# Optimization experiments

Hardware: AMD Instinct MI355X
Metric: run time of the kernel (lower is better)

## Reference

```python
import jax, jax.numpy as jnp
import numpy as np

BLOCK_H = 32
BLOCK_W = 32
HEADS = 16
SEQ = 1024
BATCH = 8
HEAD_DIM = 64


def _block_mask(mask):
    # conv with all-ones kernel, stride = block size, grouped per head == block sum-pool, then >0
    H, S, Sw = mask.shape
    nb_h, nb_w = S // BLOCK_H, Sw // BLOCK_W
    pooled = mask.reshape(H, nb_h, BLOCK_H, nb_w, BLOCK_W).sum(axis=(2, 4))
    return pooled > 0  # [H, nb_h, nb_w] bool


def setup_inputs() -> dict:
    key = jax.random.key(0)
    kq, kk, kv, km = jax.random.split(key, 4)
    q = jax.random.normal(kq, (BATCH, HEADS, SEQ, HEAD_DIM), dtype=jnp.float32)
    k = jax.random.normal(kk, (BATCH, HEADS, SEQ, HEAD_DIM), dtype=jnp.float32)
    v = jax.random.normal(kv, (BATCH, HEADS, SEQ, HEAD_DIM), dtype=jnp.float32)
    # with diagonal blocks always present (valid causal layout, matches triton usage).
    nb = SEQ // BLOCK_H
    bm = jax.random.uniform(km, (HEADS, nb, nb)) < 0.25
    bm = bm | jnp.eye(nb, dtype=bool)[None, :, :]
    # expand block mask to element-level float mask [H, S, S]
    mask = jnp.broadcast_to(
        bm[:, :, None, :, None], (HEADS, nb, BLOCK_H, nb, BLOCK_W)
    ).reshape(HEADS, SEQ, SEQ).astype(jnp.float32)
    return {"query": q, "key": k, "value": v, "mask": mask}


def reference(query, key, value, mask):
    scale = 1.0
    bm = _block_mask(mask)  # [H, nb, nb]
    nb = bm.shape[-1]
    # expand block layout back to element granularity (triton masks per-block only)
    elem = jnp.broadcast_to(
        bm[:, :, None, :, None], (bm.shape[0], nb, BLOCK_H, nb, BLOCK_W)
    ).reshape(bm.shape[0], nb * BLOCK_H, nb * BLOCK_W)
    causal = jnp.tril(jnp.ones((elem.shape[-2], elem.shape[-1]), dtype=bool))
    full = elem & causal[None]  # [H, S, S]
    # SDD: QK^T only on layout blocks; dense equivalent masks to -inf elsewhere
    scores = jnp.einsum("bhqd,bhkd->bhqk", query, key) * scale
    scores = jnp.where(full[None], scores, -jnp.inf)
    probs = jax.nn.softmax(scores, axis=-1)  # every row has a valid diagonal-block entry
    # DSD: sparse probs @ dense V
    out = jnp.einsum("bhqk,bhkd->bhqd", probs, value)
    return out
```

## Files before the change

kernel.cpp:

```cpp
#include <hip/hip_runtime.h>
#include <stdint.h>

typedef unsigned short u16;
typedef short bf16x8 __attribute__((ext_vector_type(8)));
typedef bf16x8 __attribute__((may_alias)) bf16x8_a;
typedef unsigned u32x2 __attribute__((ext_vector_type(2)));
typedef u32x2 __attribute__((may_alias)) u32x2_a;
typedef float f32x4 __attribute__((ext_vector_type(4)));
typedef f32x4 __attribute__((may_alias)) f32x4_a;

#define BATCH 8
#define HEADS 16
#define SEQ 1024
#define HD 64
#define NB 32
#define LOG2E 1.44269504f
#define MBIAS 46.16624128f
#define BLK 2048

__device__ unsigned g_bm[HEADS * NB];
__device__ u16 g_kb[(size_t)BATCH * HEADS * NB * BLK];
__device__ u16 g_kl[(size_t)BATCH * HEADS * NB * BLK];
__device__ u16 g_vt[(size_t)BATCH * HEADS * NB * BLK];

__device__ __forceinline__ u16 f2bf(float x) {
    unsigned u = __builtin_bit_cast(unsigned, x);
    u += 0x7fffu + ((u >> 16) & 1u);
    return (u16)(u >> 16);
}
__device__ __forceinline__ float bf2f(u16 h) {
    unsigned u = ((unsigned)h) << 16;
    return __builtin_bit_cast(float, u);
}
__device__ __forceinline__ bf16x8 pack8(float4 a, float4 b) {
    bf16x8 r;
    r[0] = (short)f2bf(a.x); r[1] = (short)f2bf(a.y);
    r[2] = (short)f2bf(a.z); r[3] = (short)f2bf(a.w);
    r[4] = (short)f2bf(b.x); r[5] = (short)f2bf(b.y);
    r[6] = (short)f2bf(b.z); r[7] = (short)f2bf(b.w);
    return r;
}
__device__ __forceinline__ bf16x8 pack8_res(float4 a, float4 b, bf16x8 hi) {
    bf16x8 r;
    r[0] = (short)f2bf(a.x - bf2f((u16)hi[0])); r[1] = (short)f2bf(a.y - bf2f((u16)hi[1]));
    r[2] = (short)f2bf(a.z - bf2f((u16)hi[2])); r[3] = (short)f2bf(a.w - bf2f((u16)hi[3]));
    r[4] = (short)f2bf(b.x - bf2f((u16)hi[4])); r[5] = (short)f2bf(b.y - bf2f((u16)hi[5]));
    r[6] = (short)f2bf(b.z - bf2f((u16)hi[6])); r[7] = (short)f2bf(b.w - bf2f((u16)hi[7]));
    return r;
}

__global__ __launch_bounds__(256) void prep_kv(const float* __restrict__ k,
                                               const float* __restrict__ v,
                                               const float* __restrict__ mask) {
    __shared__ float tile[64 * 65];
    int bid = blockIdx.x;
    int t = threadIdx.x;
    if (bid < 4096) {
        int bh = bid >> 5, j = bid & 31;
        int row = t >> 3, dg = t & 7;
        const float* s = k + ((size_t)(bh * SEQ + j * 32 + row)) * HD + dg * 8;
        float4 a = *(const float4*)(s);
        float4 b = *(const float4*)(s + 4);
        bf16x8 hi = pack8(a, b);
        bf16x8 lo = pack8_res(a, b, hi);
        int c = ((row >> 4) << 1) + (dg >> 2);
        int lane = (row & 15) + ((dg & 3) << 4);
        size_t o = ((size_t)(bh * NB + j)) * BLK + c * 512 + lane * 8;
        *(bf16x8*)(g_kb + o) = hi;
        *(bf16x8*)(g_kl + o) = lo;
        return;
    }
    if (bid < 6144) {
        int tb = bid - 4096;
        int bh = tb >> 4, kt = tb & 15;
        const float* src = v + ((size_t)(bh * SEQ + kt * 64)) * HD;
#pragma unroll
        for (int p = 0; p < 4; ++p) {
            int row = p * 16 + (t >> 4);
            int col = (t & 15) * 4;
            float4 d = *(const float4*)(src + (size_t)row * HD + col);
            float* tp = &tile[row * 65 + col];
            tp[0] = d.x; tp[1] = d.y; tp[2] = d.z; tp[3] = d.w;
        }
        __syncthreads();
#pragma unroll
        for (int p = 0; p < 2; ++p) {
            int dd = p * 32 + (t >> 3);
            int kc = (t & 7) * 8;
            u16 tmp[8];
#pragma unroll
            for (int i = 0; i < 8; ++i) tmp[i] = f2bf(tile[(kc + i) * 65 + dd]);
            int j = kt * 2 + (kc >> 5);
            int kk = kc & 31;
            int c = dd >> 4;
            int lane = (dd & 15) + ((kk >> 3) << 4);
            size_t o = ((size_t)(bh * NB + j)) * BLK + c * 512 + lane * 8;
            *(uint4*)(g_vt + o) = *(const uint4*)tmp;
        }
        return;
    }
    int h = bid - 6144;
    int lane = t & 63;
#pragma unroll
    for (int kk2 = 0; kk2 < 4; ++kk2) {
        int tt = (kk2 << 8) | t;
        int i = tt >> 5, j = tt & 31;
        float mv = mask[(size_t)h * SEQ * SEQ + (size_t)(i * 32) * SEQ + (size_t)(j * 32)];
        bool pred = (j == i) || (j < i && mv != 0.0f);
        unsigned long long bal = __ballot(pred);
        if (lane == 0)  g_bm[h * NB + i] = (unsigned)(bal & 0xffffffffull);
        if (lane == 32) g_bm[h * NB + i] = (unsigned)(bal >> 32);
    }
}

__device__ __forceinline__ void load_blk(size_t kb, bf16x8 (&kh)[4], bf16x8 (&kl)[4],
                                         bf16x8 (&vf)[4]) {
#pragma unroll
    for (int c = 0; c < 4; ++c) {
        kh[c] = *(const bf16x8_a*)(const void*)(g_kb + kb + c * 512);
        kl[c] = *(const bf16x8_a*)(const void*)(g_kl + kb + c * 512);
        vf[c] = *(const bf16x8_a*)(const void*)(g_vt + kb + c * 512);
    }
}

__device__ __forceinline__ void compute_blk(int j, int i32, int qcol, int quad,
                                            const bf16x8 (&kh)[4], const bf16x8 (&kl)[4],
                                            const bf16x8 (&vf)[4],
                                            const bf16x8 (&qh)[2][2], const bf16x8 (&ql)[2][2],
                                            u16* pl, f32x4 (&oacc)[2][4], float& l0, float& l1) {
    f32x4 tt[2][2];
    __builtin_amdgcn_s_setprio(1);
#pragma unroll
    for (int kt = 0; kt < 2; ++kt)
#pragma unroll
        for (int t = 0; t < 2; ++t) {
            f32x4 acc = f32x4{0.f, 0.f, 0.f, 0.f};
            acc = __builtin_amdgcn_mfma_f32_16x16x32_bf16(kl[kt*2+0], qh[t][0], acc, 0, 0, 0);
            acc = __builtin_amdgcn_mfma_f32_16x16x32_bf16(kl[kt*2+1], qh[t][1], acc, 0, 0, 0);
            acc = __builtin_amdgcn_mfma_f32_16x16x32_bf16(kh[kt*2+0], ql[t][0], acc, 0, 0, 0);
            acc = __builtin_amdgcn_mfma_f32_16x16x32_bf16(kh[kt*2+1], ql[t][1], acc, 0, 0, 0);
            acc = __builtin_amdgcn_mfma_f32_16x16x32_bf16(kh[kt*2+0], qh[t][0], acc, 0, 0, 0);
            acc = __builtin_amdgcn_mfma_f32_16x16x32_bf16(kh[kt*2+1], qh[t][1], acc, 0, 0, 0);
            tt[kt][t] = acc;
        }
    __builtin_amdgcn_s_setprio(0);

    if (j == i32) {
#pragma unroll
        for (int kt = 0; kt < 2; ++kt)
#pragma unroll
            for (int t = 0; t < 2; ++t)
#pragma unroll
                for (int r = 0; r < 4; ++r) {
                    int key = kt * 16 + quad * 4 + r;
                    if (key > t * 16 + qcol) tt[kt][t][r] = -1e30f;
                }
    }

    u16 pb[2][8];
#pragma unroll
    for (int kt = 0; kt < 2; ++kt)
#pragma unroll
        for (int t = 0; t < 2; ++t) {
            float psum = 0.f;
#pragma unroll
            for (int r = 0; r < 4; ++r) {
                float e = exp2f(tt[kt][t][r] * LOG2E - MBIAS);
                u16 eb = f2bf(e);
                pb[t][kt * 4 + r] = eb;
                psum += bf2f(eb);
            }
            if (t == 0) l0 += psum; else l1 += psum;
        }

#pragma unroll
    for (int t = 0; t < 2; ++t)
#pragma unroll
        for (int kt = 0; kt < 2; ++kt) {
            u32x2 pw;
            pw[0] = (unsigned)pb[t][kt*4+0] | ((unsigned)pb[t][kt*4+1] << 16);
            pw[1] = (unsigned)pb[t][kt*4+2] | ((unsigned)pb[t][kt*4+3] << 16);
            *(u32x2_a*)(pl + (t * 16 + qcol) * 40 + kt * 16 + quad * 4) = pw;
        }
    bf16x8 pf0 = *(const bf16x8_a*)(pl + qcol * 40 + quad * 8);
    bf16x8 pf1 = *(const bf16x8_a*)(pl + (16 + qcol) * 40 + quad * 8);

    __builtin_amdgcn_s_setprio(1);
#pragma unroll
    for (int c = 0; c < 4; ++c) {
        oacc[0][c] = __builtin_amdgcn_mfma_f32_16x16x32_bf16(vf[c], pf0, oacc[0][c], 0, 0, 0);
        oacc[1][c] = __builtin_amdgcn_mfma_f32_16x16x32_bf16(vf[c], pf1, oacc[1][c], 0, 0, 0);
    }
    __builtin_amdgcn_s_setprio(0);
}

__global__ __launch_bounds__(128) void attn(const float* __restrict__ q,
                                            float* __restrict__ out) {
    __shared__ __align__(16) u16 pbuf[2][1280];
    __shared__ __align__(16) float mbuf[2176];
    __shared__ float lbuf[2][16];

    int w = threadIdx.x >> 6;
    int lane = threadIdx.x & 63;
    int qcol = lane & 15;
    int quad = lane >> 4;

    int bid = blockIdx.x;
    int slot = bid & 7;
    int r = bid >> 3;
    int half = r >> 8;
    int rr = r & 255;
    int i32 = 31 - (rr >> 3);
    int bh = slot + ((((half << 3) | (rr & 7))) << 3);
    int h = bh & (HEADS - 1);

    bf16x8 qh[2][2], ql[2][2];
#pragma unroll
    for (int t = 0; t < 2; ++t) {
        const float* qb = q + ((size_t)(bh * SEQ + i32 * 32 + t * 16 + qcol)) * HD + quad * 8;
#pragma unroll
        for (int dh = 0; dh < 2; ++dh) {
            float4 a = *(const float4*)(qb + dh * 32);
            float4 b = *(const float4*)(qb + dh * 32 + 4);
            qh[t][dh] = pack8(a, b);
            ql[t][dh] = pack8_res(a, b, qh[t][dh]);
        }
    }

    unsigned bits = g_bm[h * NB + i32];
    unsigned mybits = 0;
    {
        unsigned b = bits; int c = 0;
        while (b) { int j = __builtin_ctz(b); b &= b - 1; if ((c & 1) == w) mybits |= (1u << j); ++c; }
    }

    size_t bhbase = (size_t)bh * NB * BLK + lane * 8;
    u16* pl = pbuf[w];

    f32x4 oacc[2][4];
#pragma unroll
    for (int t = 0; t < 2; ++t)
#pragma unroll
        for (int c = 0; c < 4; ++c) oacc[t][c] = f32x4{0.f, 0.f, 0.f, 0.f};
    float l0 = 0.f, l1 = 0.f;

    bf16x8 khA[4], klA[4], vfA[4], khB[4], klB[4], vfB[4];
    unsigned rem = mybits;
    if (rem) {
        int jA = __builtin_ctz(rem); rem &= rem - 1;
        load_blk(bhbase + (size_t)jA * BLK, khA, klA, vfA);
        for (;;) {
            int jB = -1;
            if (rem) { jB = __builtin_ctz(rem); rem &= rem - 1;
                       load_blk(bhbase + (size_t)jB * BLK, khB, klB, vfB); }
            compute_blk(jA, i32, qcol, quad, khA, klA, vfA, qh, ql, pl, oacc, l0, l1);
            if (jB < 0) break;
            jA = -1;
            if (rem) { jA = __builtin_ctz(rem); rem &= rem - 1;
                       load_blk(bhbase + (size_t)jA * BLK, khA, klA, vfA); }
            compute_blk(jB, i32, qcol, quad, khB, klB, vfB, qh, ql, pl, oacc, l0, l1);
            if (jA < 0) break;
        }
    }

    l0 += __shfl_xor(l0, 16); l0 += __shfl_xor(l0, 32);
    l1 += __shfl_xor(l1, 16); l1 += __shfl_xor(l1, 32);

    if (w == 1) {
#pragma unroll
        for (int t = 0; t < 2; ++t)
#pragma unroll
            for (int c = 0; c < 4; ++c) {
                f32x4 val;
                val[0] = oacc[t][c][0]; val[1] = oacc[t][c][1];
                val[2] = oacc[t][c][2]; val[3] = oacc[t][c][3];
                *(f32x4_a*)(&mbuf[(t * 16 + qcol) * 68 + c * 16 + quad * 4]) = val;
            }
        if (quad == 0) { lbuf[0][qcol] = l0; lbuf[1][qcol] = l1; }
    }
    __syncthreads();
    if (w == 0) {
        float inv[2];
        inv[0] = 1.0f / (l0 + lbuf[0][qcol]);
        inv[1] = 1.0f / (l1 + lbuf[1][qcol]);
#pragma unroll
        for (int t = 0; t < 2; ++t)
#pragma unroll
            for (int c = 0; c < 4; ++c) {
                float* mp = &mbuf[(t * 16 + qcol) * 68 + c * 16 + quad * 4];
                f32x4 o = *(const f32x4_a*)mp;
                o[0] = (o[0] + oacc[t][c][0]) * inv[t];
                o[1] = (o[1] + oacc[t][c][1]) * inv[t];
                o[2] = (o[2] + oacc[t][c][2]) * inv[t];
                o[3] = (o[3] + oacc[t][c][3]) * inv[t];
                *(f32x4_a*)mp = o;
            }
    }
    __syncthreads();
    float* obase = out + ((size_t)(bh * SEQ + i32 * 32)) * HD;
#pragma unroll
    for (int g2 = 0; g2 < 4; ++g2) {
        int gr = w * 4 + g2;
        int row = gr * 4 + (lane >> 4);
        int colf = (lane & 15) * 4;
        f32x4 val = *(const f32x4_a*)(&mbuf[row * 68 + colf]);
        *(float4*)(obase + (size_t)row * HD + colf) = make_float4(val[0], val[1], val[2], val[3]);
    }
}

extern "C" void kernel_launch(void* const* d_in, const int* in_sizes, int n_in,
                              void* d_out, int out_size, void* d_ws, size_t ws_size,
                              hipStream_t stream) {
    const float* q = (const float*)d_in[0];
    const float* k = (const float*)d_in[1];
    const float* v = (const float*)d_in[2];
    const float* mask = (const float*)d_in[3];
    float* out = (float*)d_out;

    prep_kv<<<4096 + 2048 + 16, 256, 0, stream>>>(k, v, mask);
    attn<<<4096, 128, 0, stream>>>(q, out);
}
```

Baseline: 203.4 us.

## Use single-wave attention blocks and halve V-transpose shared tile

The attention kernel drops from two waves per block, each handling alternate key blocks, to one wave that walks every active key block. This removes the cross-wave merge through shared memory and both block barriers at the end, and it frees shared memory and raises blocks per CU. The cost is less parallelism within a block and longer serial work per wave. The V transpose in prep_kv now runs in two 32-row passes over a half-size tile, with an extra barrier per pass.

Result: no change. 203.5 us (+0.1%).

```diff
diff --git a/kernel.cpp b/kernel.cpp
--- a/kernel.cpp
+++ b/kernel.cpp
@@ -52,7 +52,7 @@
 __global__ __launch_bounds__(256) void prep_kv(const float* __restrict__ k,
                                                const float* __restrict__ v,
                                                const float* __restrict__ mask) {
-    __shared__ float tile[64 * 65];
+    __shared__ float tile[32 * 65];
     int bid = blockIdx.x;
     int t = threadIdx.x;
     if (bid < 4096) {
@@ -75,27 +75,29 @@
         int bh = tb >> 4, kt = tb & 15;
         const float* src = v + ((size_t)(bh * SEQ + kt * 64)) * HD;
 #pragma unroll
-        for (int p = 0; p < 4; ++p) {
-            int row = p * 16 + (t >> 4);
-            int col = (t & 15) * 4;
-            float4 d = *(const float4*)(src + (size_t)row * HD + col);
-            float* tp = &tile[row * 65 + col];
-            tp[0] = d.x; tp[1] = d.y; tp[2] = d.z; tp[3] = d.w;
-        }
-        __syncthreads();
-#pragma unroll
-        for (int p = 0; p < 2; ++p) {
-            int dd = p * 32 + (t >> 3);
-            int kc = (t & 7) * 8;
-            u16 tmp[8];
-#pragma unroll
-            for (int i = 0; i < 8; ++i) tmp[i] = f2bf(tile[(kc + i) * 65 + dd]);
-            int j = kt * 2 + (kc >> 5);
-            int kk = kc & 31;
-            int c = dd >> 4;
-            int lane = (dd & 15) + ((kk >> 3) << 4);
-            size_t o = ((size_t)(bh * NB + j)) * BLK + c * 512 + lane * 8;
-            *(uint4*)(g_vt + o) = *(const uint4*)tmp;
+        for (int pass = 0; pass < 2; ++pass) {
+#pragma unroll
+            for (int p = 0; p < 2; ++p) {
+                int row = p * 16 + (t >> 4);
+                int col = (t & 15) * 4;
+                float4 d = *(const float4*)(src + (size_t)(pass * 32 + row) * HD + col);
+                float* tp = &tile[row * 65 + col];
+                tp[0] = d.x; tp[1] = d.y; tp[2] = d.z; tp[3] = d.w;
+            }
+            __syncthreads();
+            {
+                int dd = t >> 2;
+                int kc = (t & 3) * 8;
+                u16 tmp[8];
+#pragma unroll
+                for (int i = 0; i < 8; ++i) tmp[i] = f2bf(tile[(kc + i) * 65 + dd]);
+                int j = kt * 2 + pass;
+                int c = dd >> 4;
+                int lane = (dd & 15) + ((kc >> 3) << 4);
+                size_t o = ((size_t)(bh * NB + j)) * BLK + c * 512 + lane * 8;
+                *(uint4*)(g_vt + o) = *(const uint4*)tmp;
+            }
+            __syncthreads();
         }
         return;
     }
@@ -194,13 +196,10 @@
     __builtin_amdgcn_s_setprio(0);
 }
 
-__global__ __launch_bounds__(128) void attn(const float* __restrict__ q,
-                                            float* __restrict__ out) {
-    __shared__ __align__(16) u16 pbuf[2][1280];
-    __shared__ __align__(16) float mbuf[2176];
-    __shared__ float lbuf[2][16];
-
-    int w = threadIdx.x >> 6;
+__global__ __launch_bounds__(64) void attn(const float* __restrict__ q,
+                                           float* __restrict__ out) {
+    __shared__ __align__(16) char smem[8704];
+
     int lane = threadIdx.x & 63;
     int qcol = lane & 15;
     int quad = lane >> 4;
@@ -228,14 +227,8 @@
     }
 
     unsigned bits = g_bm[h * NB + i32];
-    unsigned mybits = 0;
-    {
-        unsigned b = bits; int c = 0;
-        while (b) { int j = __builtin_ctz(b); b &= b - 1; if ((c & 1) == w) mybits |= (1u << j); ++c; }
-    }
-
     size_t bhbase = (size_t)bh * NB * BLK + lane * 8;
-    u16* pl = pbuf[w];
+    u16* pl = (u16*)smem;
 
     f32x4 oacc[2][4];
 #pragma unroll
@@ -245,7 +238,7 @@
     float l0 = 0.f, l1 = 0.f;
 
     bf16x8 khA[4], klA[4], vfA[4], khB[4], klB[4], vfB[4];
-    unsigned rem = mybits;
+    unsigned rem = bits;
     if (rem) {
         int jA = __builtin_ctz(rem); rem &= rem - 1;
         load_blk(bhbase + (size_t)jA * BLK, khA, klA, vfA);
@@ -265,45 +258,24 @@
 
     l0 += __shfl_xor(l0, 16); l0 += __shfl_xor(l0, 32);
     l1 += __shfl_xor(l1, 16); l1 += __shfl_xor(l1, 32);
-
-    if (w == 1) {
-#pragma unroll
-        for (int t = 0; t < 2; ++t)
-#pragma unroll
-            for (int c = 0; c < 4; ++c) {
-                f32x4 val;
-                val[0] = oacc[t][c][0]; val[1] = oacc[t][c][1];
-                val[2] = oacc[t][c][2]; val[3] = oacc[t][c][3];
-                *(f32x4_a*)(&mbuf[(t * 16 + qcol) * 68 + c * 16 + quad * 4]) = val;
-            }
-        if (quad == 0) { lbuf[0][qcol] = l0; lbuf[1][qcol] = l1; }
-    }
-    __syncthreads();
-    if (w == 0) {
-        float inv[2];
-        inv[0] = 1.0f / (l0 + lbuf[0][qcol]);
-        inv[1] = 1.0f / (l1 + lbuf[1][qcol]);
-#pragma unroll
-        for (int t = 0; t < 2; ++t)
-#pragma unroll
-            for (int c = 0; c < 4; ++c) {
-                float* mp = &mbuf[(t * 16 + qcol) * 68 + c * 16 + quad * 4];
-                f32x4 o = *(const f32x4_a*)mp;
-                o[0] = (o[0] + oacc[t][c][0]) * inv[t];
-                o[1] = (o[1] + oacc[t][c][1]) * inv[t];
-                o[2] = (o[2] + oacc[t][c][2]) * inv[t];
-                o[3] = (o[3] + oacc[t][c][3]) * inv[t];
-                *(f32x4_a*)mp = o;
-            }
-    }
-    __syncthreads();
+    float inv[2] = {1.0f / l0, 1.0f / l1};
+
+    float* ol = (float*)smem;
+#pragma unroll
+    for (int t = 0; t < 2; ++t)
+#pragma unroll
+        for (int c = 0; c < 4; ++c) {
+            f32x4 val;
+            val[0] = oacc[t][c][0] * inv[t]; val[1] = oacc[t][c][1] * inv[t];
+            val[2] = oacc[t][c][2] * inv[t]; val[3] = oacc[t][c][3] * inv[t];
+            *(f32x4_a*)(ol + (t * 16 + qcol) * 68 + c * 16 + quad * 4) = val;
+        }
     float* obase = out + ((size_t)(bh * SEQ + i32 * 32)) * HD;
 #pragma unroll
-    for (int g2 = 0; g2 < 4; ++g2) {
-        int gr = w * 4 + g2;
+    for (int gr = 0; gr < 8; ++gr) {
         int row = gr * 4 + (lane >> 4);
         int colf = (lane & 15) * 4;
-        f32x4 val = *(const f32x4_a*)(&mbuf[row * 68 + colf]);
+        f32x4 val = *(const f32x4_a*)(ol + row * 68 + colf);
         *(float4*)(obase + (size_t)row * HD + colf) = make_float4(val[0], val[1], val[2], val[3]);
     }
 }
@@ -318,5 +290,5 @@
     float* out = (float*)d_out;
 
     prep_kv<<<4096 + 2048 + 16, 256, 0, stream>>>(k, v, mask);
-    attn<<<4096, 128, 0, stream>>>(q, out);
-}
+    attn<<<4096, 64, 0, stream>>>(q, out);
+}
```
